# Kernel optimization log

Hardware: AMD Instinct MI355X
Metric: run time of the kernel (lower is better)

The kernel has to match this reference:

```python
import jax, jax.numpy as jnp
import numpy as np

N_NODES = 100000
N_EDGES = 1600000
D_IN = 128
D_OUT = 128


def setup_inputs() -> dict:
    key = jax.random.key(0)
    k_x, k_e, k_wl, k_bl, k_wr = jax.random.split(key, 5)
    x = jax.random.normal(k_x, (N_NODES, D_IN), dtype=jnp.float32)
    edge_index = jax.random.randint(k_e, (2, N_EDGES), 0, N_NODES, dtype=jnp.int64)
    s = 1.0 / np.sqrt(D_IN)
    W_l = jax.random.uniform(k_wl, (D_OUT, D_IN), minval=-s, maxval=s, dtype=jnp.float32)
    b_l = jax.random.uniform(k_bl, (D_OUT,), minval=-s, maxval=s, dtype=jnp.float32)
    W_r = jax.random.uniform(k_wr, (D_OUT, D_IN), minval=-s, maxval=s, dtype=jnp.float32)
    return {"x": x, "edge_index": edge_index, "W_l": W_l, "b_l": b_l, "W_r": W_r}


def reference(x, edge_index, W_l, b_l, W_r):
    # PyG SAGEConv with mean aggregation:
    #   out = lin_l(mean_{j in N(i)} x_j) + lin_r(x_i), followed by ReLU.
    src, dst = edge_index[0], edge_index[1]
    # gather source features [E, D_IN] and mean-aggregate at destinations
    msg_sum = jax.ops.segment_sum(x[src], dst, num_segments=N_NODES)  # [N, D_IN]
    deg = jax.ops.segment_sum(jnp.ones((edge_index.shape[1],), dtype=x.dtype), dst,
                              num_segments=N_NODES)  # [N]
    agg = msg_sum / jnp.maximum(deg, 1.0)[:, None]  # isolated nodes -> 0
    out = agg @ W_l.T + b_l + x @ W_r.T
    return jax.nn.relu(out)
```

## Files before the change

### kernel.cpp

```cpp
#include <hip/hip_runtime.h>
#include <hip/hip_bf16.h>
#include <cstddef>
#include <cstdint>

#define D 128
#define BCAP 262144
#define BCHUNK 4096
#define SLOTS 64
#define TILE 128
#define LROW 68
#define SBCAP 5120
#define GPGMAX 64

typedef __bf16 bf16x8 __attribute__((ext_vector_type(8)));
typedef float  f32x4  __attribute__((ext_vector_type(4)));
typedef float  f32x2  __attribute__((ext_vector_type(2)));

__device__ __forceinline__ unsigned int f2bf(float f) {
    unsigned int u = __float_as_uint(f);
    return (u + 0x7FFFu + ((u >> 16) & 1u)) >> 16;
}

__global__ __launch_bounds__(256) void bucketx_kernel(
    const int* __restrict__ ei, int E, int* __restrict__ bucketCnt,
    int2* __restrict__ buckets, int nbBucket, int nbX,
    const float4* __restrict__ x4, uint2* __restrict__ xb2,
    unsigned int* __restrict__ xg, int nq,
    const float* __restrict__ Wl, const float* __restrict__ Wr,
    const float* __restrict__ bl, unsigned short* __restrict__ bfrag,
    float* __restrict__ biasbuf)
{
    const int bid = blockIdx.x;
    if (bid >= nbBucket) {
        const int xi = bid - nbBucket;
        if (xi < nbX) {
            const int base = xi * 1024 + threadIdx.x;
            #pragma unroll
            for (int k = 0; k < 4; k++) {
                int i = base + k * 256;
                if (i < nq) {
                    float4 v = x4[i];
                    uint2 r;
                    r.x = f2bf(v.x) | (f2bf(v.y) << 16);
                    r.y = f2bf(v.z) | (f2bf(v.w) << 16);
                    xb2[i] = r;
                    int g = 0;
                    g = __builtin_amdgcn_cvt_pk_fp8_f32(v.x, v.y, g, false);
                    g = __builtin_amdgcn_cvt_pk_fp8_f32(v.z, v.w, g, true);
                    xg[(size_t)((i >> 5) + 1) * 32 + (i & 31)] = (unsigned int)g;
                }
            }
        } else {
            int f = (xi - nbX) * 256 + threadIdx.x;
            if (f < 4096) {
                int ct   = f >> 9;
                int q    = (f >> 6) & 7;
                int lane = f & 63;
                int o  = 16 * ct + (lane & 15);
                int kb = 32 * q + (lane >> 4) * 8;
                const float* s = (kb < 128) ? (Wl + (size_t)o * 128 + kb)
                                            : (Wr + (size_t)o * 128 + (kb - 128));
                uint4 u;
                u.x = f2bf(s[0]) | (f2bf(s[1]) << 16);
                u.y = f2bf(s[2]) | (f2bf(s[3]) << 16);
                u.z = f2bf(s[4]) | (f2bf(s[5]) << 16);
                u.w = f2bf(s[6]) | (f2bf(s[7]) << 16);
                reinterpret_cast<uint4*>(bfrag)[f] = u;
                if (f < 128) biasbuf[f] = bl[f];
                if (f < 32)  xg[f] = 0u;
            }
        }
        return;
    }
    __shared__ int cnt[8], base[8], pos[8];
    const int cb  = bid * BCHUNK;
    const int end = min(cb + BCHUNK, E);
    if (threadIdx.x < 8) { cnt[threadIdx.x] = 0; pos[threadIdx.x] = 0; }
    __syncthreads();
    int srcs[16], dsts[16];
    #pragma unroll
    for (int k = 0; k < 16; k++) {
        int e = cb + threadIdx.x + k * 256;
        bool v = e < end;
        srcs[k] = v ? ei[e] : 0;
        dsts[k] = v ? ei[E + e] : -1;
        if (v) atomicAdd(&cnt[(dsts[k] >> 8) & 7], 1);
    }
    __syncthreads();
    if (threadIdx.x < 8)
        base[threadIdx.x] = atomicAdd(&bucketCnt[threadIdx.x], cnt[threadIdx.x]);
    __syncthreads();
    #pragma unroll
    for (int k = 0; k < 16; k++) {
        if (dsts[k] >= 0) {
            int p = (dsts[k] >> 8) & 7;
            int o = base[p] + atomicAdd(&pos[p], 1);
            if (o < BCAP) buckets[(size_t)p * BCAP + o] = make_int2(srcs[k], dsts[k]);
        }
    }
}

__global__ __launch_bounds__(256) void granule_kernel(
    const int2* __restrict__ buckets, const int* __restrict__ bucketCnt,
    int* __restrict__ subCnt, unsigned int* __restrict__ sub, int GPG)
{
    __shared__ int cnt[GPGMAX], base[GPGMAX], posl[GPGMAX];
    const int p = blockIdx.x & 7;
    const int j = blockIdx.x >> 3;
    const int n = min(bucketCnt[p], BCAP);
    const int lo = j * 4096;
    if (lo >= n) return;
    const int hi = min(lo + 4096, n);
    for (int i = threadIdx.x; i < GPG; i += 256) { cnt[i] = 0; posl[i] = 0; }
    __syncthreads();
    const int2* B = buckets + (size_t)p * BCAP;
    int2 e[16]; int gi[16];
    #pragma unroll
    for (int k = 0; k < 16; k++) {
        int i = lo + threadIdx.x + k * 256;
        bool v = i < hi;
        e[k] = v ? B[i] : make_int2(0, 0);
        gi[k] = v ? (e[k].y >> 11) : -1;
        if (v) atomicAdd(&cnt[gi[k]], 1);
    }
    __syncthreads();
    for (int i = threadIdx.x; i < GPG; i += 256)
        base[i] = (cnt[i] > 0) ? atomicAdd(&subCnt[p * GPG + i], cnt[i]) : 0;
    __syncthreads();
    #pragma unroll
    for (int k = 0; k < 16; k++) {
        if (gi[k] >= 0) {
            int pos = base[gi[k]] + atomicAdd(&posl[gi[k]], 1);
            if (pos < SBCAP)
                sub[(size_t)(p * GPG + gi[k]) * SBCAP + pos] =
                    (unsigned int)(e[k].x + 1) | ((unsigned int)(e[k].y & 255) << 20);
        }
    }
}

__global__ __launch_bounds__(256) void csrg_kernel(
    const unsigned int* __restrict__ sub, const int* __restrict__ subCnt,
    int* __restrict__ csr, int* __restrict__ deg, int GPG, int N)
{
    __shared__ int lcnt[256];
    const int g  = blockIdx.x;
    const int p  = g & 7;
    const int gi = g >> 3;
    const int sb = p * GPG + gi;
    const int n  = min(subCnt[sb], SBCAP);
    lcnt[threadIdx.x] = 0;
    __syncthreads();
    const unsigned int* S = sub + (size_t)sb * SBCAP;
    const int nbase = g << 8;
    for (int i = threadIdx.x; i < n; i += 256) {
        unsigned int en = S[i];
        int d8  = (en >> 20) & 255;
        int pos = atomicAdd(&lcnt[d8], 1);
        if (pos < SLOTS)
            csr[(size_t)(nbase + d8) * SLOTS + pos] = (int)(en & 0xFFFFFu);
    }
    __syncthreads();
    int node = nbase + threadIdx.x;
    if (node < N) deg[node] = lcnt[threadIdx.x];
}

__global__ __launch_bounds__(512) void gathformer_kernel(
    const int* __restrict__ deg_, const int* __restrict__ csr,
    const unsigned int* __restrict__ xg, const unsigned int* __restrict__ xb,
    const unsigned short* __restrict__ bfrag, const float* __restrict__ biasbuf,
    float* __restrict__ out, int N)
{
    __shared__ unsigned int lds[TILE * LROW];

    const int w    = threadIdx.x >> 6;
    const int lane = threadIdx.x & 63;
    const int sub  = lane & 31;
    const int half = lane >> 5;
    const int node0 = blockIdx.x * TILE;

    for (int i = 0; i < 16; i++) {
        int node = node0 + w * 16 + i;
        if (node >= N) break;
        int deg = deg_[node];
        int dl  = min(deg, SLOTS);
        int nbatch = (dl + 15) >> 4;
        const int* nb = csr + (size_t)node * SLOTS;
        f32x2 a01 = {0.f, 0.f};
        f32x2 a23 = {0.f, 0.f};
        for (int b = 0; b < nbatch; b++) {
            const int j = b * 16;
            unsigned int v[8];
            #pragma unroll
            for (int u = 0; u < 8; u++) {
                int slot = j + 2 * u + half;
                int raw  = nb[slot];
                int s    = (slot < dl) ? raw : 0;
                v[u] = xg[(size_t)s * 32 + sub];
            }
            #pragma unroll
            for (int u = 0; u < 8; u++) {
                a01 += __builtin_amdgcn_cvt_pk_f32_fp8(v[u], false);
                a23 += __builtin_amdgcn_cvt_pk_f32_fp8(v[u], true);
            }
        }
        a01.x += __shfl_xor(a01.x, 32);
        a01.y += __shfl_xor(a01.y, 32);
        a23.x += __shfl_xor(a23.x, 32);
        a23.y += __shfl_xor(a23.y, 32);
        if (half == 0) {
            float inv = 1.0f / fmaxf((float)deg, 1.0f);
            int b = (w * 16 + i) * LROW + sub * 2;
            lds[b]     = f2bf(a01.x * inv) | (f2bf(a01.y * inv) << 16);
            lds[b + 1] = f2bf(a23.x * inv) | (f2bf(a23.y * inv) << 16);
        }
    }
    __syncthreads();

    const int quad = lane >> 4;
    const int r15  = lane & 15;
    bf16x8 bw[8];
    #pragma unroll
    for (int q = 0; q < 8; q++)
        bw[q] = reinterpret_cast<const bf16x8*>(bfrag)[(w * 8 + q) * 64 + lane];
    const float bias = biasbuf[16 * w + r15];
    const int col = 16 * w + r15;

    #pragma unroll 1
    for (int mt = 0; mt < 8; mt++) {
        int rowbase = node0 + mt * 16;
        if (rowbase >= N) break;
        int rc = min(rowbase + r15, N - 1);
        f32x4 acc = {0.f, 0.f, 0.f, 0.f};
        const int lbase = (mt * 16 + r15) * LROW + quad * 4;
        #pragma unroll
        for (int q = 0; q < 4; q++) {
            bf16x8 a = *reinterpret_cast<const bf16x8*>(&lds[lbase + q * 16]);
            acc = __builtin_amdgcn_mfma_f32_16x16x32_bf16(a, bw[q], acc, 0, 0, 0);
        }
        const unsigned short* xrow =
            (const unsigned short*)xb + (size_t)rc * 128 + quad * 8;
        #pragma unroll
        for (int q = 4; q < 8; q++) {
            bf16x8 a = *reinterpret_cast<const bf16x8*>(xrow + (q - 4) * 32);
            acc = __builtin_amdgcn_mfma_f32_16x16x32_bf16(a, bw[q], acc, 0, 0, 0);
        }
        #pragma unroll
        for (int r = 0; r < 4; r++) {
            int orow = rowbase + quad * 4 + r;
            if (orow < N)
                out[(size_t)orow * D + col] = fmaxf(acc[r] + bias, 0.0f);
        }
    }
}

extern "C" void kernel_launch(void* const* d_in, const int* in_sizes, int n_in,
                              void* d_out, int out_size, void* d_ws, size_t ws_size,
                              hipStream_t stream)
{
    const float* x  = (const float*)d_in[0];
    const int*   ei = (const int*)d_in[1];
    const float* Wl = (const float*)d_in[2];
    const float* bl = (const float*)d_in[3];
    const float* Wr = (const float*)d_in[4];
    float* out = (float*)d_out;

    const int nodes = in_sizes[0] / D;
    const int E     = in_sizes[1] / 2;
    const int NG    = (nodes + 255) >> 8;
    const int GPG   = (NG + 7) >> 3;

    int* deg         = (int*)d_ws;
    unsigned int* xg = (unsigned int*)(deg + nodes);
    int* csr         = (int*)(xg + (size_t)(nodes + 1) * 32);
    unsigned int* xb = (unsigned int*)(csr + (size_t)nodes * SLOTS);
    unsigned short* bfrag = (unsigned short*)(xb + (size_t)nodes * 64);
    float* biasbuf   = (float*)(bfrag + 4096 * 8);
    int* bucketCnt   = (int*)(biasbuf + 128);
    int* subCnt      = bucketCnt + 8;
    int2* buckets    = (int2*)d_out;
    unsigned int* sub = (unsigned int*)((char*)d_out + (size_t)8 * BCAP * 8);

    hipMemsetAsync(bucketCnt, 0, (size_t)(8 + 8 * GPG) * sizeof(int), stream);

    const int nbBucket = (E + BCHUNK - 1) / BCHUNK;
    const int nq  = nodes * 32;
    const int nbX = (nq + 1023) / 1024;
    bucketx_kernel<<<nbBucket + nbX + 16, 256, 0, stream>>>(
        ei, E, bucketCnt, buckets, nbBucket, nbX,
        (const float4*)x, (uint2*)xb, xg, nq, Wl, Wr, bl, bfrag, biasbuf);

    const int PB = (BCAP + 4095) / 4096;
    granule_kernel<<<8 * PB, 256, 0, stream>>>(buckets, bucketCnt, subCnt, sub, GPG);

    csrg_kernel<<<NG, 256, 0, stream>>>(sub, subCnt, csr, deg, GPG, nodes);

    gathformer_kernel<<<(nodes + TILE - 1) / TILE, 512, 0, stream>>>(
        deg, csr, xg, xb, bfrag, biasbuf, out, nodes);
}
```

Measured before the change: 221.8 us.

## Use wave-ballot bucketing, halve gather tile, and shuffle-broadcast neighbor lists

```diff
diff --git a/kernel.cpp b/kernel.cpp
--- a/kernel.cpp
+++ b/kernel.cpp
@@ -7,7 +7,7 @@
 #define BCAP 262144
 #define BCHUNK 4096
 #define SLOTS 64
-#define TILE 128
+#define TILE 64
 #define LROW 68
 #define SBCAP 5120
 #define GPGMAX 64
@@ -72,30 +72,40 @@
         }
         return;
     }
-    __shared__ int cnt[8], base[8], pos[8];
-    const int cb  = bid * BCHUNK;
-    const int end = min(cb + BCHUNK, E);
-    if (threadIdx.x < 8) { cnt[threadIdx.x] = 0; pos[threadIdx.x] = 0; }
-    __syncthreads();
-    int srcs[16], dsts[16];
-    #pragma unroll
-    for (int k = 0; k < 16; k++) {
-        int e = cb + threadIdx.x + k * 256;
-        bool v = e < end;
-        srcs[k] = v ? ei[e] : 0;
-        dsts[k] = v ? ei[E + e] : -1;
-        if (v) atomicAdd(&cnt[(dsts[k] >> 8) & 7], 1);
-    }
-    __syncthreads();
-    if (threadIdx.x < 8)
-        base[threadIdx.x] = atomicAdd(&bucketCnt[threadIdx.x], cnt[threadIdx.x]);
-    __syncthreads();
-    #pragma unroll
-    for (int k = 0; k < 16; k++) {
-        if (dsts[k] >= 0) {
-            int p = (dsts[k] >> 8) & 7;
-            int o = base[p] + atomicAdd(&pos[p], 1);
-            if (o < BCAP) buckets[(size_t)p * BCAP + o] = make_int2(srcs[k], dsts[k]);
+    const int lane = threadIdx.x & 63;
+    const int wv   = threadIdx.x >> 6;
+    const unsigned long long lt = (1ULL << lane) - 1ULL;
+    const int cb   = bid * BCHUNK + wv * 1024;
+    const int end  = min(bid * BCHUNK + BCHUNK, E);
+
+    int sk[16], dk[16], pk[16], sl[16];
+    #pragma unroll
+    for (int k = 0; k < 16; k++) {
+        int i = cb + k * 64 + lane;
+        bool v = i < end;
+        sk[k] = v ? ei[i] : 0;
+        dk[k] = v ? ei[E + i] : 0;
+        pk[k] = v ? ((dk[k] >> 8) & 7) : -1;
+    }
+    int cw[8] = {0, 0, 0, 0, 0, 0, 0, 0};
+    #pragma unroll
+    for (int k = 0; k < 16; k++) {
+        #pragma unroll
+        for (int part = 0; part < 8; part++) {
+            unsigned long long m = __ballot(pk[k] == part);
+            if (pk[k] == part) sl[k] = cw[part] + __popcll(m & lt);
+            cw[part] += __popcll(m);
+        }
+    }
+    int mybase = 0;
+    if (lane < 8) mybase = atomicAdd(&bucketCnt[lane], cw[lane]);
+    #pragma unroll
+    for (int k = 0; k < 16; k++) {
+        int b = __shfl(mybase, pk[k] < 0 ? 0 : pk[k]);
+        if (pk[k] >= 0) {
+            int o = b + sl[k];
+            if (o < BCAP)
+                buckets[(size_t)pk[k] * BCAP + o] = make_int2(sk[k], dk[k]);
         }
     }
 }
@@ -178,13 +188,19 @@
     const int half = lane >> 5;
     const int node0 = blockIdx.x * TILE;
 
-    for (int i = 0; i < 16; i++) {
-        int node = node0 + w * 16 + i;
+    int degs[8];
+    #pragma unroll
+    for (int i = 0; i < 8; i++) {
+        int node = node0 + w * 8 + i;
+        degs[i] = (node < N) ? deg_[node] : 0;
+    }
+    for (int i = 0; i < 8; i++) {
+        int node = node0 + w * 8 + i;
         if (node >= N) break;
-        int deg = deg_[node];
+        int deg = degs[i];
         int dl  = min(deg, SLOTS);
         int nbatch = (dl + 15) >> 4;
-        const int* nb = csr + (size_t)node * SLOTS;
+        int nbrow = csr[(size_t)node * SLOTS + lane];
         f32x2 a01 = {0.f, 0.f};
         f32x2 a23 = {0.f, 0.f};
         for (int b = 0; b < nbatch; b++) {
@@ -193,7 +209,7 @@
             #pragma unroll
             for (int u = 0; u < 8; u++) {
                 int slot = j + 2 * u + half;
-                int raw  = nb[slot];
+                int raw  = __shfl(nbrow, slot);
                 int s    = (slot < dl) ? raw : 0;
                 v[u] = xg[(size_t)s * 32 + sub];
             }
@@ -209,7 +225,7 @@
         a23.y += __shfl_xor(a23.y, 32);
         if (half == 0) {
             float inv = 1.0f / fmaxf((float)deg, 1.0f);
-            int b = (w * 16 + i) * LROW + sub * 2;
+            int b = (w * 8 + i) * LROW + sub * 2;
             lds[b]     = f2bf(a01.x * inv) | (f2bf(a01.y * inv) << 16);
             lds[b + 1] = f2bf(a23.x * inv) | (f2bf(a23.y * inv) << 16);
         }
@@ -226,7 +242,7 @@
     const int col = 16 * w + r15;
 
     #pragma unroll 1
-    for (int mt = 0; mt < 8; mt++) {
+    for (int mt = 0; mt < 4; mt++) {
         int rowbase = node0 + mt * 16;
         if (rowbase >= N) break;
         int rc = min(rowbase + r15, N - 1);
```

Result: no change. 224.2 us (+1.1%).
